# Kernel tuning notes

Measured on AMD Instinct MI355X. Metric: run time of the kernel, lower is better.

## Reference

```python
import jax, jax.numpy as jnp
import numpy as np

B, T, D, NQ, NK, H = 2, 2048, 2048, 16, 4, 128
ROPE_THETA = 10000.0

def _timescale(head_dim, max_ts=ROPE_THETA, min_ts=1.0):
    frac = 2.0 * jnp.arange(head_dim // 2, dtype=jnp.float32) / head_dim
    return (min_ts * (max_ts / min_ts) ** frac).astype(jnp.float32)

def _apply_rope(x, pos):
    # x: [B,S,N,H], pos: [B,S] int
    ts = _timescale(x.shape[-1])
    sinu = pos.astype(jnp.float32)[..., None, None] / ts  # [B,S,1,H/2]
    sin, cos = jnp.sin(sinu), jnp.cos(sinu)
    x = x.astype(jnp.float32)
    x1, x2 = jnp.split(x, 2, axis=-1)
    return jnp.concatenate((x1 * cos - x2 * sin, x2 * cos + x1 * sin), axis=-1)

def setup_inputs() -> dict:
    key = jax.random.key(0)
    ks = jax.random.split(key, 5)
    X = jax.random.normal(ks[0], (B, T, D), dtype=jnp.float32)
    q_positions = jnp.broadcast_to(jnp.arange(T, dtype=jnp.int32), (B, T))
    s = 1.0 / np.sqrt(D)
    Wq = jax.random.normal(ks[1], (D, NQ, H), dtype=jnp.float32) * s
    Wk = jax.random.normal(ks[2], (D, NK, H), dtype=jnp.float32) * s
    Wv = jax.random.normal(ks[3], (D, NK, H), dtype=jnp.float32) * s
    Wo = jax.random.normal(ks[4], (NQ, H, D), dtype=jnp.float32) * (1.0 / np.sqrt(NQ * H))
    return {"X": X, "q_positions": q_positions, "Wq": Wq, "Wk": Wk, "Wv": Wv, "Wo": Wo}

def reference(X, q_positions, Wq, Wk, Wv, Wo):
    # Q/K/V projections
    q = jnp.einsum('btd,dnh->btnh', X, Wq)   # [B,T,NQ,H]
    k = jnp.einsum('bsd,dkh->bskh', X, Wk)   # [B,S,NK,H]
    v = jnp.einsum('bsd,dkh->bskh', X, Wv)
    # RoPE (kv_positions defaults to q_positions)
    q = _apply_rope(q, q_positions)
    k = _apply_rope(k, q_positions)
    # GQA causal SDPA, scale=1.0 (as in source)
    G = NQ // NK
    qg = q.reshape(B, T, NK, G, H)
    logits = jnp.einsum('btkgh,bskh->bkgts', qg, k)  # [B,NK,G,T,S]
    t_idx = jnp.arange(T)[:, None]
    s_idx = jnp.arange(T)[None, :]
    causal = (s_idx <= t_idx)
    logits = jnp.where(causal, logits, jnp.finfo(logits.dtype).min)
    probs = jax.nn.softmax(logits, axis=-1)
    attn = jnp.einsum('bkgts,bskh->btkgh', probs, v).reshape(B, T, NQ, H)
    out = jnp.einsum('btnh,nhd->btd', attn, Wo)
    return out.astype(X.dtype)
```

## Files before the change

### kernel.cpp

```cpp
#include <hip/hip_runtime.h>


typedef _Float16 half8 __attribute__((ext_vector_type(8)));
typedef _Float16 half4 __attribute__((ext_vector_type(4)));
typedef float f32x4 __attribute__((ext_vector_type(4)));

#define GLOAD16(gp, lp) \
  __builtin_amdgcn_global_load_lds((__attribute__((address_space(1))) void*)(gp), \
                                   (__attribute__((address_space(3))) void*)(lp), 16, 0, 0)

#define WAIT_VM8() asm volatile("s_waitcnt vmcnt(8)" ::: "memory")
#define WAIT_VM0() asm volatile("s_waitcnt vmcnt(0)" ::: "memory")
#define BAR() asm volatile("s_barrier" ::: "memory")

static constexpr int T_   = 2048;
static constexpr int D_   = 2048;
static constexpr int NQ_  = 16;
static constexpr int NK_  = 4;
static constexpr int H_   = 128;
static constexpr int NQKV = 3072;
static constexpr int KOFF = 2048;
static constexpr int VOFF = 2560;


__global__ void cast_x_kernel(const float* __restrict__ in, _Float16* __restrict__ out) {
  int i = (blockIdx.x * 256 + threadIdx.x) * 4;
  float4 v = *reinterpret_cast<const float4*>(in + i);
  union { _Float16 h[4]; uint2 u; } p;
  p.h[0] = (_Float16)v.x; p.h[1] = (_Float16)v.y;
  p.h[2] = (_Float16)v.z; p.h[3] = (_Float16)v.w;
  *reinterpret_cast<uint2*>(out + i) = p.u;
}

__global__ void transpose_cast_kernel(const float* __restrict__ in,
                                      _Float16* __restrict__ out, int ncols) {
  __shared__ float tile[32][33];
  int n0 = blockIdx.x * 32, k0 = blockIdx.y * 32;
  int tx = threadIdx.x, ty = threadIdx.y;
#pragma unroll
  for (int i = 0; i < 32; i += 8)
    tile[ty + i][tx] = in[(size_t)(k0 + ty + i) * ncols + (n0 + tx)];
  __syncthreads();
#pragma unroll
  for (int i = 0; i < 32; i += 8)
    out[(size_t)(n0 + ty + i) * 2048 + (k0 + tx)] = (_Float16)tile[tx][ty + i];
}

__global__ void rope_kernel(_Float16* __restrict__ qkv, const int* __restrict__ pos) {
  int idx = blockIdx.x * 256 + threadIdx.x;
  int h = idx & 63;
  int head = (idx >> 6) % 20;
  int m = idx / (64 * 20);
  float p = (float)pos[m];
  float freq = expf(-0.14391156831f * (float)h);
  float a = p * freq;
  float s, c;
  sincosf(a, &s, &c);
  int col = (head < 16) ? (head * H_ + h) : (KOFF + (head - 16) * H_ + h);
  _Float16* ptr = qkv + (size_t)m * NQKV + col;
  float x1 = (float)ptr[0], x2 = (float)ptr[64];
  ptr[0]  = (_Float16)(x1 * c - x2 * s);
  ptr[64] = (_Float16)(x2 * c + x1 * s);
}

__global__ void vtrans_kernel(const _Float16* __restrict__ qkv, _Float16* __restrict__ vt) {
  __shared__ _Float16 tile[32][33];
  int t0 = blockIdx.x * 32, h0 = blockIdx.y * 32;
  int slab = blockIdx.z;
  int tx = threadIdx.x, ty = threadIdx.y;
  int b = slab >> 2, kh = slab & 3;
#pragma unroll
  for (int i = 0; i < 32; i += 8)
    tile[ty + i][tx] = qkv[(size_t)(b * T_ + t0 + ty + i) * NQKV + VOFF + kh * H_ + h0 + tx];
  __syncthreads();
#pragma unroll
  for (int i = 0; i < 32; i += 8)
    vt[(size_t)(slab * H_ + h0 + ty + i) * T_ + (t0 + tx)] = tile[tx][ty + i];
}


template <int OUT_F32>
__global__ __launch_bounds__(256, 2) void gemm_kernel(const _Float16* __restrict__ A,
                                                      const _Float16* __restrict__ Bt,
                                                      void* __restrict__ Cout, int N, int K) {
  __shared__ __align__(16) _Float16 As[128 * 64];
  __shared__ __align__(16) _Float16 Bs[128 * 64];
  const int tid = threadIdx.x;
  const int wave = tid >> 6, lane = tid & 63;
  const int lg = lane >> 4, lm = lane & 15;
  const int brow = blockIdx.y * 128, bcol = blockIdx.x * 128;
  const int wr = wave >> 1, wc = wave & 1;
  f32x4 acc[4][4] = {};
  for (int k0 = 0; k0 < K; k0 += 64) {
#pragma unroll
    for (int j = 0; j < 4; ++j) {
      int U = j * 256 + tid;
      int row = U >> 3, u = U & 7;
      int us = u ^ (row & 7);
      GLOAD16(A + (size_t)(brow + row) * K + k0 + us * 8, (char*)As + ((j * 256 + wave * 64) << 4));
      GLOAD16(Bt + (size_t)(bcol + row) * K + k0 + us * 8, (char*)Bs + ((j * 256 + wave * 64) << 4));
    }
    __syncthreads();
#pragma unroll
    for (int kk = 0; kk < 2; ++kk) {
      half8 af[4], bf[4];
#pragma unroll
      for (int m = 0; m < 4; ++m) {
        int row = wr * 64 + m * 16 + lm;
        int u = (kk * 4 + lg) ^ (row & 7);
        af[m] = *reinterpret_cast<const half8*>(As + row * 64 + u * 8);
      }
#pragma unroll
      for (int n = 0; n < 4; ++n) {
        int row = wc * 64 + n * 16 + lm;
        int u = (kk * 4 + lg) ^ (row & 7);
        bf[n] = *reinterpret_cast<const half8*>(Bs + row * 64 + u * 8);
      }
#pragma unroll
      for (int m = 0; m < 4; ++m)
#pragma unroll
        for (int n = 0; n < 4; ++n)
          acc[m][n] = __builtin_amdgcn_mfma_f32_16x16x32_f16(af[m], bf[n], acc[m][n], 0, 0, 0);
    }
    __syncthreads();
  }
#pragma unroll
  for (int m = 0; m < 4; ++m)
#pragma unroll
    for (int n = 0; n < 4; ++n)
#pragma unroll
      for (int r = 0; r < 4; ++r) {
        size_t row = brow + wr * 64 + m * 16 + lg * 4 + r;
        size_t col = bcol + wc * 64 + n * 16 + lm;
        if constexpr (OUT_F32) ((float*)Cout)[row * N + col] = acc[m][n][r];
        else ((_Float16*)Cout)[row * N + col] = (_Float16)acc[m][n][r];
      }
}


__global__ __launch_bounds__(256, 2) void attn_kernel(const _Float16* __restrict__ qkv,
                                                      const _Float16* __restrict__ vt,
                                                      _Float16* __restrict__ attn) {
  __shared__ __align__(16) _Float16 Ks[2][64 * 128];
  __shared__ __align__(16) _Float16 Vs[2][128 * 64];
  __shared__ __align__(16) _Float16 Ps[4][16 * 64];
  const int bid = blockIdx.x;
  const int swz = (bid & 7) * 64 + (bid >> 3);
  const int chunk = swz >> 6;
  const int b = chunk >> 2, kh = chunk & 3;
  const int n = kh * 4 + ((swz >> 4) & 3);
  const int p = swz & 15;
  const int tid = threadIdx.x, wave = tid >> 6, lane = tid & 63;
  const int lg = lane >> 4, lm = lane & 15;

  auto stage = [&](int j, int buf) {
    const int s0 = j * 64;
    char* Kb = (char*)&Ks[buf][0];
    char* Vb = (char*)&Vs[buf][0];
#pragma unroll
    for (int jj = 0; jj < 4; ++jj) {
      int U = jj * 256 + tid;
      int srow = U >> 4, u = U & 15;
      int us = u ^ (srow & 15);
      GLOAD16(qkv + (size_t)(b * T_ + s0 + srow) * NQKV + KOFF + kh * H_ + us * 8,
              Kb + ((jj * 256 + wave * 64) << 4));
    }
#pragma unroll
    for (int jj = 0; jj < 4; ++jj) {
      int U = jj * 256 + tid;
      int hrow = U >> 3, u = U & 7;
      int us = u ^ (hrow & 7);
      GLOAD16(vt + (size_t)((b * NK_ + kh) * H_ + hrow) * T_ + s0 + us * 8,
              Vb + ((jj * 256 + wave * 64) << 4));
    }
  };

  for (int ph = 0; ph < 2; ++ph) {
    const int t = ph ? (31 - p) : p;
    const int qbase = t * 64 + wave * 16;

    half8 qf[4];
    const _Float16* qptr = qkv + (size_t)(b * T_ + qbase + lm) * NQKV + n * H_;
#pragma unroll
    for (int kk = 0; kk < 4; ++kk) {
      half8 qr = *reinterpret_cast<const half8*>(qptr + kk * 32 + lg * 8);
#pragma unroll
      for (int j = 0; j < 8; ++j)
        qf[kk][j] = (_Float16)((float)qr[j] * 1.4426950408889634f);
    }

    f32x4 o[8] = {};
    float mrow_s = -1e30f, lrow_s = 0.f;

    const int nkv = t + 1;
    stage(0, 0);
    for (int it = 0; it < nkv; ++it) {
      const int cur = it & 1;
      if (it + 1 < nkv) { stage(it + 1, cur ^ 1); WAIT_VM8(); }
      else              { WAIT_VM0(); }
      BAR();
      const _Float16* Kt = &Ks[cur][0];
      const _Float16* Vt2 = &Vs[cur][0];

      f32x4 S[4];
      __builtin_amdgcn_s_setprio(1);
#pragma unroll
      for (int ns = 0; ns < 4; ++ns) {
        half8 kf[4];
        int srow = ns * 16 + lm;
#pragma unroll
        for (int kk = 0; kk < 4; ++kk) {
          int u = (kk * 4 + lg) ^ (srow & 15);
          kf[kk] = *reinterpret_cast<const half8*>(Kt + srow * 128 + u * 8);
        }
        f32x4 a = {0.f, 0.f, 0.f, 0.f};
#pragma unroll
        for (int kk = 0; kk < 4; ++kk)
          a = __builtin_amdgcn_mfma_f32_16x16x32_f16(kf[kk], qf[kk], a, 0, 0, 0);
        S[ns] = a;
      }
      __builtin_amdgcn_s_setprio(0);

      if (it == t) {
        const int q = qbase + lm;
#pragma unroll
        for (int ns = 0; ns < 4; ++ns)
#pragma unroll
          for (int r = 0; r < 4; ++r) {
            int s = t * 64 + ns * 16 + lg * 4 + r;
            if (s > q) S[ns][r] = -1e30f;
          }
      }

      float pm0 = fmaxf(fmaxf(S[0][0], S[0][1]), fmaxf(S[0][2], S[0][3]));
      float pm1 = fmaxf(fmaxf(S[1][0], S[1][1]), fmaxf(S[1][2], S[1][3]));
      float pm2 = fmaxf(fmaxf(S[2][0], S[2][1]), fmaxf(S[2][2], S[2][3]));
      float pm3 = fmaxf(fmaxf(S[3][0], S[3][1]), fmaxf(S[3][2], S[3][3]));
      float pm = fmaxf(fmaxf(pm0, pm1), fmaxf(pm2, pm3));
      pm = fmaxf(pm, __shfl_xor(pm, 16));
      pm = fmaxf(pm, __shfl_xor(pm, 32));

      if (__any(pm > mrow_s + 14.f)) {
        float mn = fmaxf(mrow_s, pm);
        float sc = __builtin_amdgcn_exp2f(mrow_s - mn);
        mrow_s = mn;
        lrow_s *= sc;
        float scr[4];
#pragma unroll
        for (int r = 0; r < 4; ++r) scr[r] = __shfl(sc, lg * 4 + r);
#pragma unroll
        for (int nh = 0; nh < 8; ++nh)
#pragma unroll
          for (int r = 0; r < 4; ++r) o[nh][r] *= scr[r];
      }

      const float m = mrow_s;
      float ps = 0.f;
#pragma unroll
      for (int ns = 0; ns < 4; ++ns)
#pragma unroll
        for (int r = 0; r < 4; ++r) {
          float pv = __builtin_amdgcn_exp2f(S[ns][r] - m);
          S[ns][r] = pv;
          ps += pv;
        }
      ps += __shfl_xor(ps, 16);
      ps += __shfl_xor(ps, 32);
      lrow_s += ps;

#pragma unroll
      for (int ns = 0; ns < 4; ++ns) {
        half4 pk;
#pragma unroll
        for (int r = 0; r < 4; ++r) pk[r] = (_Float16)S[ns][r];
        int u = (2 * ns + (lg >> 1)) ^ (lm & 7);
        *reinterpret_cast<half4*>(&Ps[wave][lm * 64 + u * 8 + (lg & 1) * 4]) = pk;
      }

      __builtin_amdgcn_s_setprio(1);
#pragma unroll
      for (int kk2 = 0; kk2 < 2; ++kk2) {
        int up = (kk2 * 4 + lg) ^ (lm & 7);
        half8 pa = *reinterpret_cast<const half8*>(&Ps[wave][lm * 64 + up * 8]);
#pragma unroll
        for (int nh = 0; nh < 8; ++nh) {
          int hrow = nh * 16 + lm;
          int u = (kk2 * 4 + lg) ^ (hrow & 7);
          half8 vf = *reinterpret_cast<const half8*>(Vt2 + hrow * 64 + u * 8);
          o[nh] = __builtin_amdgcn_mfma_f32_16x16x32_f16(pa, vf, o[nh], 0, 0, 0);
        }
      }
      __builtin_amdgcn_s_setprio(0);
      BAR();
    }

    float linv[4];
#pragma unroll
    for (int r = 0; r < 4; ++r) linv[r] = 1.f / __shfl(lrow_s, lg * 4 + r);
#pragma unroll
    for (int r = 0; r < 4; ++r) {
      int q = qbase + lg * 4 + r;
      _Float16* optr = attn + ((size_t)(b * T_ + q) * NQ_ + n) * H_ + lm;
#pragma unroll
      for (int nh = 0; nh < 8; ++nh)
        optr[nh * 16] = (_Float16)(o[nh][r] * linv[r]);
    }
  }
}


extern "C" void kernel_launch(void* const* d_in, const int* in_sizes, int n_in,
                              void* d_out, int out_size, void* d_ws, size_t ws_size,
                              hipStream_t stream) {
  const float* X  = (const float*)d_in[0];
  const int* pos  = (const int*)d_in[1];
  const float* Wq = (const float*)d_in[2];
  const float* Wk = (const float*)d_in[3];
  const float* Wv = (const float*)d_in[4];
  const float* Wo = (const float*)d_in[5];

  _Float16* Xh    = (_Float16*)d_ws;
  _Float16* Wqkvt = Xh + (size_t)4096 * 2048;
  _Float16* Wot   = Wqkvt + (size_t)3072 * 2048;
  _Float16* QKV   = Wot + (size_t)2048 * 2048;
  _Float16* Vt    = QKV + (size_t)4096 * 3072;
  _Float16* Attn  = Vt + (size_t)8 * 128 * 2048;

  dim3 tb(32, 8);
  cast_x_kernel<<<8192, 256, 0, stream>>>(X, Xh);
  transpose_cast_kernel<<<dim3(64, 64), tb, 0, stream>>>(Wq, Wqkvt, 2048);
  transpose_cast_kernel<<<dim3(16, 64), tb, 0, stream>>>(Wk, Wqkvt + (size_t)2048 * 2048, 512);
  transpose_cast_kernel<<<dim3(16, 64), tb, 0, stream>>>(Wv, Wqkvt + (size_t)2560 * 2048, 512);
  transpose_cast_kernel<<<dim3(64, 64), tb, 0, stream>>>(Wo, Wot, 2048);

  gemm_kernel<0><<<dim3(24, 32), 256, 0, stream>>>(Xh, Wqkvt, QKV, NQKV, 2048);
  rope_kernel<<<20480, 256, 0, stream>>>(QKV, pos);
  vtrans_kernel<<<dim3(64, 4, 8), tb, 0, stream>>>(QKV, Vt);
  attn_kernel<<<512, 256, 0, stream>>>(QKV, Vt, Attn);
  gemm_kernel<1><<<dim3(16, 32), 256, 0, stream>>>(Attn, Wot, d_out, 2048, 2048);
}
```

Before: 209.0 us.

## Process 32 query rows per wave in attention to reuse K/V tiles

The attention kernel now gives each wave two 16-row query sub-tiles, so each block covers 128 queries instead of 64. Every K and V fragment read from LDS then feeds twice as many MFMAs, and each staged K/V tile serves twice as many query rows. The grid is halved to 256 blocks, launch bounds drop to one block per CU, and the causal mask now applies to the last two KV tiles. The cost is higher register pressure, lower occupancy, and fewer blocks, which may leave part of the GPU idle given the causal load imbalance.

```diff
diff --git a/kernel.cpp b/kernel.cpp
--- a/kernel.cpp
+++ b/kernel.cpp
@@ -138,18 +138,18 @@
 }
 
 
-__global__ __launch_bounds__(256, 2) void attn_kernel(const _Float16* __restrict__ qkv,
+__global__ __launch_bounds__(256, 1) void attn_kernel(const _Float16* __restrict__ qkv,
                                                       const _Float16* __restrict__ vt,
                                                       _Float16* __restrict__ attn) {
   __shared__ __align__(16) _Float16 Ks[2][64 * 128];
   __shared__ __align__(16) _Float16 Vs[2][128 * 64];
-  __shared__ __align__(16) _Float16 Ps[4][16 * 64];
+  __shared__ __align__(16) _Float16 Ps[4][32 * 64];
   const int bid = blockIdx.x;
-  const int swz = (bid & 7) * 64 + (bid >> 3);
-  const int chunk = swz >> 6;
+  const int swz = (bid & 7) * 32 + (bid >> 3);
+  const int chunk = swz >> 5;
   const int b = chunk >> 2, kh = chunk & 3;
-  const int n = kh * 4 + ((swz >> 4) & 3);
-  const int p = swz & 15;
+  const int n = kh * 4 + ((swz >> 3) & 3);
+  const int p = swz & 7;
   const int tid = threadIdx.x, wave = tid >> 6, lane = tid & 63;
   const int lg = lane >> 4, lm = lane & 15;
 
@@ -176,23 +176,26 @@
   };
 
   for (int ph = 0; ph < 2; ++ph) {
-    const int t = ph ? (31 - p) : p;
-    const int qbase = t * 64 + wave * 16;
-
-    half8 qf[4];
-    const _Float16* qptr = qkv + (size_t)(b * T_ + qbase + lm) * NQKV + n * H_;
-#pragma unroll
-    for (int kk = 0; kk < 4; ++kk) {
-      half8 qr = *reinterpret_cast<const half8*>(qptr + kk * 32 + lg * 8);
-#pragma unroll
-      for (int j = 0; j < 8; ++j)
-        qf[kk][j] = (_Float16)((float)qr[j] * 1.4426950408889634f);
-    }
-
-    f32x4 o[8] = {};
-    float mrow_s = -1e30f, lrow_s = 0.f;
-
-    const int nkv = t + 1;
+    const int t = ph ? (15 - p) : p;
+    const int qbase = t * 128 + wave * 32;
+
+    half8 qf[2][4];
+#pragma unroll
+    for (int mq = 0; mq < 2; ++mq) {
+      const _Float16* qptr = qkv + (size_t)(b * T_ + qbase + mq * 16 + lm) * NQKV + n * H_;
+#pragma unroll
+      for (int kk = 0; kk < 4; ++kk) {
+        half8 qr = *reinterpret_cast<const half8*>(qptr + kk * 32 + lg * 8);
+#pragma unroll
+        for (int j = 0; j < 8; ++j)
+          qf[mq][kk][j] = (_Float16)((float)qr[j] * 1.4426950408889634f);
+      }
+    }
+
+    f32x4 o[2][8] = {};
+    float mrow[2] = {-1e30f, -1e30f}, lrow[2] = {0.f, 0.f};
+
+    const int nkv = 2 * t + 2;
     stage(0, 0);
     for (int it = 0; it < nkv; ++it) {
       const int cur = it & 1;
@@ -202,7 +205,7 @@
       const _Float16* Kt = &Ks[cur][0];
       const _Float16* Vt2 = &Vs[cur][0];
 
-      f32x4 S[4];
+      f32x4 S[2][4];
       __builtin_amdgcn_s_setprio(1);
 #pragma unroll
       for (int ns = 0; ns < 4; ++ns) {
@@ -213,97 +216,124 @@
           int u = (kk * 4 + lg) ^ (srow & 15);
           kf[kk] = *reinterpret_cast<const half8*>(Kt + srow * 128 + u * 8);
         }
-        f32x4 a = {0.f, 0.f, 0.f, 0.f};
-#pragma unroll
-        for (int kk = 0; kk < 4; ++kk)
-          a = __builtin_amdgcn_mfma_f32_16x16x32_f16(kf[kk], qf[kk], a, 0, 0, 0);
-        S[ns] = a;
+#pragma unroll
+        for (int mq = 0; mq < 2; ++mq) {
+          f32x4 a = {0.f, 0.f, 0.f, 0.f};
+#pragma unroll
+          for (int kk = 0; kk < 4; ++kk)
+            a = __builtin_amdgcn_mfma_f32_16x16x32_f16(kf[kk], qf[mq][kk], a, 0, 0, 0);
+          S[mq][ns] = a;
+        }
       }
       __builtin_amdgcn_s_setprio(0);
 
-      if (it == t) {
-        const int q = qbase + lm;
+      if (it >= 2 * t) {
+#pragma unroll
+        for (int mq = 0; mq < 2; ++mq) {
+          const int q = qbase + mq * 16 + lm;
+#pragma unroll
+          for (int ns = 0; ns < 4; ++ns)
+#pragma unroll
+            for (int r = 0; r < 4; ++r) {
+              int s = it * 64 + ns * 16 + lg * 4 + r;
+              if (s > q) S[mq][ns][r] = -1e30f;
+            }
+        }
+      }
+
+      float pm[2];
+#pragma unroll
+      for (int mq = 0; mq < 2; ++mq) {
+        float a0 = fmaxf(fmaxf(S[mq][0][0], S[mq][0][1]), fmaxf(S[mq][0][2], S[mq][0][3]));
+        float a1 = fmaxf(fmaxf(S[mq][1][0], S[mq][1][1]), fmaxf(S[mq][1][2], S[mq][1][3]));
+        float a2 = fmaxf(fmaxf(S[mq][2][0], S[mq][2][1]), fmaxf(S[mq][2][2], S[mq][2][3]));
+        float a3 = fmaxf(fmaxf(S[mq][3][0], S[mq][3][1]), fmaxf(S[mq][3][2], S[mq][3][3]));
+        float v = fmaxf(fmaxf(a0, a1), fmaxf(a2, a3));
+        v = fmaxf(v, __shfl_xor(v, 16));
+        v = fmaxf(v, __shfl_xor(v, 32));
+        pm[mq] = v;
+      }
+
+      if (__any(pm[0] > mrow[0] + 14.f || pm[1] > mrow[1] + 14.f)) {
+#pragma unroll
+        for (int mq = 0; mq < 2; ++mq) {
+          float mn = fmaxf(mrow[mq], pm[mq]);
+          float sc = __builtin_amdgcn_exp2f(mrow[mq] - mn);
+          mrow[mq] = mn;
+          lrow[mq] *= sc;
+          float scr[4];
+#pragma unroll
+          for (int r = 0; r < 4; ++r) scr[r] = __shfl(sc, lg * 4 + r);
+#pragma unroll
+          for (int nh = 0; nh < 8; ++nh)
+#pragma unroll
+            for (int r = 0; r < 4; ++r) o[mq][nh][r] *= scr[r];
+        }
+      }
+
+#pragma unroll
+      for (int mq = 0; mq < 2; ++mq) {
+        const float m = mrow[mq];
+        float ps = 0.f;
 #pragma unroll
         for (int ns = 0; ns < 4; ++ns)
 #pragma unroll
           for (int r = 0; r < 4; ++r) {
-            int s = t * 64 + ns * 16 + lg * 4 + r;
-            if (s > q) S[ns][r] = -1e30f;
+            float pv = __builtin_amdgcn_exp2f(S[mq][ns][r] - m);
+            S[mq][ns][r] = pv;
+            ps += pv;
           }
-      }
-
-      float pm0 = fmaxf(fmaxf(S[0][0], S[0][1]), fmaxf(S[0][2], S[0][3]));
-      float pm1 = fmaxf(fmaxf(S[1][0], S[1][1]), fmaxf(S[1][2], S[1][3]));
-      float pm2 = fmaxf(fmaxf(S[2][0], S[2][1]), fmaxf(S[2][2], S[2][3]));
-      float pm3 = fmaxf(fmaxf(S[3][0], S[3][1]), fmaxf(S[3][2], S[3][3]));
-      float pm = fmaxf(fmaxf(pm0, pm1), fmaxf(pm2, pm3));
-      pm = fmaxf(pm, __shfl_xor(pm, 16));
-      pm = fmaxf(pm, __shfl_xor(pm, 32));
-
-      if (__any(pm > mrow_s + 14.f)) {
-        float mn = fmaxf(mrow_s, pm);
-        float sc = __builtin_amdgcn_exp2f(mrow_s - mn);
-        mrow_s = mn;
-        lrow_s *= sc;
-        float scr[4];
-#pragma unroll
-        for (int r = 0; r < 4; ++r) scr[r] = __shfl(sc, lg * 4 + r);
-#pragma unroll
-        for (int nh = 0; nh < 8; ++nh)
-#pragma unroll
-          for (int r = 0; r < 4; ++r) o[nh][r] *= scr[r];
-      }
-
-      const float m = mrow_s;
-      float ps = 0.f;
-#pragma unroll
-      for (int ns = 0; ns < 4; ++ns)
-#pragma unroll
-        for (int r = 0; r < 4; ++r) {
-          float pv = __builtin_amdgcn_exp2f(S[ns][r] - m);
-          S[ns][r] = pv;
-          ps += pv;
-        }
-      ps += __shfl_xor(ps, 16);
-      ps += __shfl_xor(ps, 32);
-      lrow_s += ps;
-
-#pragma unroll
-      for (int ns = 0; ns < 4; ++ns) {
-        half4 pk;
-#pragma unroll
-        for (int r = 0; r < 4; ++r) pk[r] = (_Float16)S[ns][r];
-        int u = (2 * ns + (lg >> 1)) ^ (lm & 7);
-        *reinterpret_cast<half4*>(&Ps[wave][lm * 64 + u * 8 + (lg & 1) * 4]) = pk;
+        ps += __shfl_xor(ps, 16);
+        ps += __shfl_xor(ps, 32);
+        lrow[mq] += ps;
+
+        const int qq = mq * 16 + lm;
+#pragma unroll
+        for (int ns = 0; ns < 4; ++ns) {
+          half4 pk;
+#pragma unroll
+          for (int r = 0; r < 4; ++r) pk[r] = (_Float16)S[mq][ns][r];
+          int u = (2 * ns + (lg >> 1)) ^ (lm & 7);
+          *reinterpret_cast<half4*>(&Ps[wave][qq * 64 + u * 8 + (lg & 1) * 4]) = pk;
+        }
       }
 
       __builtin_amdgcn_s_setprio(1);
 #pragma unroll
       for (int kk2 = 0; kk2 < 2; ++kk2) {
-        int up = (kk2 * 4 + lg) ^ (lm & 7);
-        half8 pa = *reinterpret_cast<const half8*>(&Ps[wave][lm * 64 + up * 8]);
+        half8 pa[2];
+#pragma unroll
+        for (int mq = 0; mq < 2; ++mq) {
+          int up = (kk2 * 4 + lg) ^ (lm & 7);
+          pa[mq] = *reinterpret_cast<const half8*>(&Ps[wave][(mq * 16 + lm) * 64 + up * 8]);
+        }
 #pragma unroll
         for (int nh = 0; nh < 8; ++nh) {
           int hrow = nh * 16 + lm;
           int u = (kk2 * 4 + lg) ^ (hrow & 7);
           half8 vf = *reinterpret_cast<const half8*>(Vt2 + hrow * 64 + u * 8);
-          o[nh] = __builtin_amdgcn_mfma_f32_16x16x32_f16(pa, vf, o[nh], 0, 0, 0);
+#pragma unroll
+          for (int mq = 0; mq < 2; ++mq)
+            o[mq][nh] = __builtin_amdgcn_mfma_f32_16x16x32_f16(pa[mq], vf, o[mq][nh], 0, 0, 0);
         }
       }
       __builtin_amdgcn_s_setprio(0);
       BAR();
     }
 
-    float linv[4];
-#pragma unroll
-    for (int r = 0; r < 4; ++r) linv[r] = 1.f / __shfl(lrow_s, lg * 4 + r);
-#pragma unroll
-    for (int r = 0; r < 4; ++r) {
-      int q = qbase + lg * 4 + r;
-      _Float16* optr = attn + ((size_t)(b * T_ + q) * NQ_ + n) * H_ + lm;
-#pragma unroll
-      for (int nh = 0; nh < 8; ++nh)
-        optr[nh * 16] = (_Float16)(o[nh][r] * linv[r]);
+#pragma unroll
+    for (int mq = 0; mq < 2; ++mq) {
+      float linv[4];
+#pragma unroll
+      for (int r = 0; r < 4; ++r) linv[r] = 1.f / __shfl(lrow[mq], lg * 4 + r);
+#pragma unroll
+      for (int r = 0; r < 4; ++r) {
+        int q = qbase + mq * 16 + lg * 4 + r;
+        _Float16* optr = attn + ((size_t)(b * T_ + q) * NQ_ + n) * H_ + lm;
+#pragma unroll
+        for (int nh = 0; nh < 8; ++nh)
+          optr[nh * 16] = (_Float16)(o[mq][nh][r] * linv[r]);
+      }
     }
   }
 }
@@ -336,6 +366,6 @@
   gemm_kernel<0><<<dim3(24, 32), 256, 0, stream>>>(Xh, Wqkvt, QKV, NQKV, 2048);
   rope_kernel<<<20480, 256, 0, stream>>>(QKV, pos);
   vtrans_kernel<<<dim3(64, 4, 8), tb, 0, stream>>>(QKV, Vt);
-  attn_kernel<<<512, 256, 0, stream>>>(QKV, Vt, Attn);
+  attn_kernel<<<256, 256, 0, stream>>>(QKV, Vt, Attn);
   gemm_kernel<1><<<dim3(16, 32), 256, 0, stream>>>(Attn, Wot, d_out, 2048, 2048);
 }
```

New measurement: 222.3 us. 6.4% more time.

## Split attention into one query tile per block and single-buffer K/V for occupancy

Applied to the files above, without the earlier changes.

The attention kernel now launches 1024 blocks, each handling one 64-row query tile instead of a paired light/heavy tile. The K/V LDS double buffer is replaced by a single buffer, and launch bounds are raised so four blocks fit per CU. The aim is to hide memory latency through more resident waves rather than through software prefetch. In exchange, each iteration now waits for its own K/V load with no overlap inside a block, and load balance relies on the interleaved ordering of causal tile sizes.

```diff
diff --git a/kernel.cpp b/kernel.cpp
--- a/kernel.cpp
+++ b/kernel.cpp
@@ -9,7 +9,6 @@
   __builtin_amdgcn_global_load_lds((__attribute__((address_space(1))) void*)(gp), \
                                    (__attribute__((address_space(3))) void*)(lp), 16, 0, 0)
 
-#define WAIT_VM8() asm volatile("s_waitcnt vmcnt(8)" ::: "memory")
 #define WAIT_VM0() asm volatile("s_waitcnt vmcnt(0)" ::: "memory")
 #define BAR() asm volatile("s_barrier" ::: "memory")
 
@@ -138,32 +137,34 @@
 }
 
 
-__global__ __launch_bounds__(256, 2) void attn_kernel(const _Float16* __restrict__ qkv,
+__global__ __launch_bounds__(256, 4) void attn_kernel(const _Float16* __restrict__ qkv,
                                                       const _Float16* __restrict__ vt,
                                                       _Float16* __restrict__ attn) {
-  __shared__ __align__(16) _Float16 Ks[2][64 * 128];
-  __shared__ __align__(16) _Float16 Vs[2][128 * 64];
+  __shared__ __align__(16) _Float16 Ks[64 * 128];
+  __shared__ __align__(16) _Float16 Vs[128 * 64];
   __shared__ __align__(16) _Float16 Ps[4][16 * 64];
   const int bid = blockIdx.x;
-  const int swz = (bid & 7) * 64 + (bid >> 3);
-  const int chunk = swz >> 6;
+  const int v = (bid & 7) * 128 + (bid >> 3);
+  const int chunk = v >> 7;
   const int b = chunk >> 2, kh = chunk & 3;
-  const int n = kh * 4 + ((swz >> 4) & 3);
-  const int p = swz & 15;
+  const int j = v & 127;
+  const int h2 = j & 3;
+  const int t_raw = j >> 2;
+  const int t = (t_raw & 1) ? (31 - (t_raw >> 1)) : (t_raw >> 1);
+  const int n = kh * 4 + h2;
   const int tid = threadIdx.x, wave = tid >> 6, lane = tid & 63;
   const int lg = lane >> 4, lm = lane & 15;
-
-  auto stage = [&](int j, int buf) {
-    const int s0 = j * 64;
-    char* Kb = (char*)&Ks[buf][0];
-    char* Vb = (char*)&Vs[buf][0];
+  const int qbase = t * 64 + wave * 16;
+
+  auto stage = [&](int it) {
+    const int s0 = it * 64;
 #pragma unroll
     for (int jj = 0; jj < 4; ++jj) {
       int U = jj * 256 + tid;
       int srow = U >> 4, u = U & 15;
       int us = u ^ (srow & 15);
       GLOAD16(qkv + (size_t)(b * T_ + s0 + srow) * NQKV + KOFF + kh * H_ + us * 8,
-              Kb + ((jj * 256 + wave * 64) << 4));
+              (char*)Ks + ((jj * 256 + wave * 64) << 4));
     }
 #pragma unroll
     for (int jj = 0; jj < 4; ++jj) {
@@ -171,140 +172,132 @@
       int hrow = U >> 3, u = U & 7;
       int us = u ^ (hrow & 7);
       GLOAD16(vt + (size_t)((b * NK_ + kh) * H_ + hrow) * T_ + s0 + us * 8,
-              Vb + ((jj * 256 + wave * 64) << 4));
+              (char*)Vs + ((jj * 256 + wave * 64) << 4));
     }
   };
 
-  for (int ph = 0; ph < 2; ++ph) {
-    const int t = ph ? (31 - p) : p;
-    const int qbase = t * 64 + wave * 16;
-
-    half8 qf[4];
-    const _Float16* qptr = qkv + (size_t)(b * T_ + qbase + lm) * NQKV + n * H_;
-#pragma unroll
-    for (int kk = 0; kk < 4; ++kk) {
-      half8 qr = *reinterpret_cast<const half8*>(qptr + kk * 32 + lg * 8);
-#pragma unroll
-      for (int j = 0; j < 8; ++j)
-        qf[kk][j] = (_Float16)((float)qr[j] * 1.4426950408889634f);
-    }
-
-    f32x4 o[8] = {};
-    float mrow_s = -1e30f, lrow_s = 0.f;
-
-    const int nkv = t + 1;
-    stage(0, 0);
-    for (int it = 0; it < nkv; ++it) {
-      const int cur = it & 1;
-      if (it + 1 < nkv) { stage(it + 1, cur ^ 1); WAIT_VM8(); }
-      else              { WAIT_VM0(); }
-      BAR();
-      const _Float16* Kt = &Ks[cur][0];
-      const _Float16* Vt2 = &Vs[cur][0];
-
-      f32x4 S[4];
-      __builtin_amdgcn_s_setprio(1);
-#pragma unroll
-      for (int ns = 0; ns < 4; ++ns) {
-        half8 kf[4];
-        int srow = ns * 16 + lm;
-#pragma unroll
-        for (int kk = 0; kk < 4; ++kk) {
-          int u = (kk * 4 + lg) ^ (srow & 15);
-          kf[kk] = *reinterpret_cast<const half8*>(Kt + srow * 128 + u * 8);
+  half8 qf[4];
+  const _Float16* qptr = qkv + (size_t)(b * T_ + qbase + lm) * NQKV + n * H_;
+#pragma unroll
+  for (int kk = 0; kk < 4; ++kk) {
+    half8 qr = *reinterpret_cast<const half8*>(qptr + kk * 32 + lg * 8);
+#pragma unroll
+    for (int jj = 0; jj < 8; ++jj)
+      qf[kk][jj] = (_Float16)((float)qr[jj] * 1.4426950408889634f);
+  }
+
+  f32x4 o[8] = {};
+  float mrow_s = -1e30f, lrow_s = 0.f;
+
+  const int nkv = t + 1;
+  stage(0);
+  for (int it = 0; it < nkv; ++it) {
+    WAIT_VM0();
+    BAR();
+
+    f32x4 S[4];
+    __builtin_amdgcn_s_setprio(1);
+#pragma unroll
+    for (int ns = 0; ns < 4; ++ns) {
+      half8 kf[4];
+      int srow = ns * 16 + lm;
+#pragma unroll
+      for (int kk = 0; kk < 4; ++kk) {
+        int u = (kk * 4 + lg) ^ (srow & 15);
+        kf[kk] = *reinterpret_cast<const half8*>(Ks + srow * 128 + u * 8);
+      }
+      f32x4 a = {0.f, 0.f, 0.f, 0.f};
+#pragma unroll
+      for (int kk = 0; kk < 4; ++kk)
+        a = __builtin_amdgcn_mfma_f32_16x16x32_f16(kf[kk], qf[kk], a, 0, 0, 0);
+      S[ns] = a;
+    }
+    __builtin_amdgcn_s_setprio(0);
+
+    if (it == t) {
+      const int q = qbase + lm;
+#pragma unroll
+      for (int ns = 0; ns < 4; ++ns)
+#pragma unroll
+        for (int r = 0; r < 4; ++r) {
+          int s = t * 64 + ns * 16 + lg * 4 + r;
+          if (s > q) S[ns][r] = -1e30f;
         }
-        f32x4 a = {0.f, 0.f, 0.f, 0.f};
-#pragma unroll
-        for (int kk = 0; kk < 4; ++kk)
-          a = __builtin_amdgcn_mfma_f32_16x16x32_f16(kf[kk], qf[kk], a, 0, 0, 0);
-        S[ns] = a;
-      }
-      __builtin_amdgcn_s_setprio(0);
-
-      if (it == t) {
-        const int q = qbase + lm;
-#pragma unroll
-        for (int ns = 0; ns < 4; ++ns)
-#pragma unroll
-          for (int r = 0; r < 4; ++r) {
-            int s = t * 64 + ns * 16 + lg * 4 + r;
-            if (s > q) S[ns][r] = -1e30f;
-          }
-      }
-
-      float pm0 = fmaxf(fmaxf(S[0][0], S[0][1]), fmaxf(S[0][2], S[0][3]));
-      float pm1 = fmaxf(fmaxf(S[1][0], S[1][1]), fmaxf(S[1][2], S[1][3]));
-      float pm2 = fmaxf(fmaxf(S[2][0], S[2][1]), fmaxf(S[2][2], S[2][3]));
-      float pm3 = fmaxf(fmaxf(S[3][0], S[3][1]), fmaxf(S[3][2], S[3][3]));
-      float pm = fmaxf(fmaxf(pm0, pm1), fmaxf(pm2, pm3));
-      pm = fmaxf(pm, __shfl_xor(pm, 16));
-      pm = fmaxf(pm, __shfl_xor(pm, 32));
-
-      if (__any(pm > mrow_s + 14.f)) {
-        float mn = fmaxf(mrow_s, pm);
-        float sc = __builtin_amdgcn_exp2f(mrow_s - mn);
-        mrow_s = mn;
-        lrow_s *= sc;
-        float scr[4];
-#pragma unroll
-        for (int r = 0; r < 4; ++r) scr[r] = __shfl(sc, lg * 4 + r);
-#pragma unroll
-        for (int nh = 0; nh < 8; ++nh)
-#pragma unroll
-          for (int r = 0; r < 4; ++r) o[nh][r] *= scr[r];
-      }
-
-      const float m = mrow_s;
-      float ps = 0.f;
-#pragma unroll
-      for (int ns = 0; ns < 4; ++ns)
-#pragma unroll
-        for (int r = 0; r < 4; ++r) {
-          float pv = __builtin_amdgcn_exp2f(S[ns][r] - m);
-          S[ns][r] = pv;
-          ps += pv;
-        }
-      ps += __shfl_xor(ps, 16);
-      ps += __shfl_xor(ps, 32);
-      lrow_s += ps;
-
-#pragma unroll
-      for (int ns = 0; ns < 4; ++ns) {
-        half4 pk;
-#pragma unroll
-        for (int r = 0; r < 4; ++r) pk[r] = (_Float16)S[ns][r];
-        int u = (2 * ns + (lg >> 1)) ^ (lm & 7);
-        *reinterpret_cast<half4*>(&Ps[wave][lm * 64 + u * 8 + (lg & 1) * 4]) = pk;
-      }
-
-      __builtin_amdgcn_s_setprio(1);
-#pragma unroll
-      for (int kk2 = 0; kk2 < 2; ++kk2) {
-        int up = (kk2 * 4 + lg) ^ (lm & 7);
-        half8 pa = *reinterpret_cast<const half8*>(&Ps[wave][lm * 64 + up * 8]);
-#pragma unroll
-        for (int nh = 0; nh < 8; ++nh) {
-          int hrow = nh * 16 + lm;
-          int u = (kk2 * 4 + lg) ^ (hrow & 7);
-          half8 vf = *reinterpret_cast<const half8*>(Vt2 + hrow * 64 + u * 8);
-          o[nh] = __builtin_amdgcn_mfma_f32_16x16x32_f16(pa, vf, o[nh], 0, 0, 0);
-        }
-      }
-      __builtin_amdgcn_s_setprio(0);
-      BAR();
-    }
-
-    float linv[4];
-#pragma unroll
-    for (int r = 0; r < 4; ++r) linv[r] = 1.f / __shfl(lrow_s, lg * 4 + r);
-#pragma unroll
-    for (int r = 0; r < 4; ++r) {
-      int q = qbase + lg * 4 + r;
-      _Float16* optr = attn + ((size_t)(b * T_ + q) * NQ_ + n) * H_ + lm;
+    }
+
+    float pm0 = fmaxf(fmaxf(S[0][0], S[0][1]), fmaxf(S[0][2], S[0][3]));
+    float pm1 = fmaxf(fmaxf(S[1][0], S[1][1]), fmaxf(S[1][2], S[1][3]));
+    float pm2 = fmaxf(fmaxf(S[2][0], S[2][1]), fmaxf(S[2][2], S[2][3]));
+    float pm3 = fmaxf(fmaxf(S[3][0], S[3][1]), fmaxf(S[3][2], S[3][3]));
+    float pm = fmaxf(fmaxf(pm0, pm1), fmaxf(pm2, pm3));
+    pm = fmaxf(pm, __shfl_xor(pm, 16));
+    pm = fmaxf(pm, __shfl_xor(pm, 32));
+
+    if (__any(pm > mrow_s + 14.f)) {
+      float mn = fmaxf(mrow_s, pm);
+      float sc = __builtin_amdgcn_exp2f(mrow_s - mn);
+      mrow_s = mn;
+      lrow_s *= sc;
+      float scr[4];
+#pragma unroll
+      for (int r = 0; r < 4; ++r) scr[r] = __shfl(sc, lg * 4 + r);
 #pragma unroll
       for (int nh = 0; nh < 8; ++nh)
-        optr[nh * 16] = (_Float16)(o[nh][r] * linv[r]);
-    }
+#pragma unroll
+        for (int r = 0; r < 4; ++r) o[nh][r] *= scr[r];
+    }
+
+    const float m = mrow_s;
+    float ps = 0.f;
+#pragma unroll
+    for (int ns = 0; ns < 4; ++ns)
+#pragma unroll
+      for (int r = 0; r < 4; ++r) {
+        float pv = __builtin_amdgcn_exp2f(S[ns][r] - m);
+        S[ns][r] = pv;
+        ps += pv;
+      }
+    ps += __shfl_xor(ps, 16);
+    ps += __shfl_xor(ps, 32);
+    lrow_s += ps;
+
+#pragma unroll
+    for (int ns = 0; ns < 4; ++ns) {
+      half4 pk;
+#pragma unroll
+      for (int r = 0; r < 4; ++r) pk[r] = (_Float16)S[ns][r];
+      int u = (2 * ns + (lg >> 1)) ^ (lm & 7);
+      *reinterpret_cast<half4*>(&Ps[wave][lm * 64 + u * 8 + (lg & 1) * 4]) = pk;
+    }
+
+    __builtin_amdgcn_s_setprio(1);
+#pragma unroll
+    for (int kk2 = 0; kk2 < 2; ++kk2) {
+      int up = (kk2 * 4 + lg) ^ (lm & 7);
+      half8 pa = *reinterpret_cast<const half8*>(&Ps[wave][lm * 64 + up * 8]);
+#pragma unroll
+      for (int nh = 0; nh < 8; ++nh) {
+        int hrow = nh * 16 + lm;
+        int u = (kk2 * 4 + lg) ^ (hrow & 7);
+        half8 vf = *reinterpret_cast<const half8*>(Vs + hrow * 64 + u * 8);
+        o[nh] = __builtin_amdgcn_mfma_f32_16x16x32_f16(pa, vf, o[nh], 0, 0, 0);
+      }
+    }
+    __builtin_amdgcn_s_setprio(0);
+    BAR();
+    if (it + 1 < nkv) stage(it + 1);
+  }
+
+  float linv[4];
+#pragma unroll
+  for (int r = 0; r < 4; ++r) linv[r] = 1.f / __shfl(lrow_s, lg * 4 + r);
+#pragma unroll
+  for (int r = 0; r < 4; ++r) {
+    int q = qbase + lg * 4 + r;
+    _Float16* optr = attn + ((size_t)(b * T_ + q) * NQ_ + n) * H_ + lm;
+#pragma unroll
+    for (int nh = 0; nh < 8; ++nh)
+      optr[nh * 16] = (_Float16)(o[nh][r] * linv[r]);
   }
 }
 
@@ -336,6 +329,6 @@
   gemm_kernel<0><<<dim3(24, 32), 256, 0, stream>>>(Xh, Wqkvt, QKV, NQKV, 2048);
   rope_kernel<<<20480, 256, 0, stream>>>(QKV, pos);
   vtrans_kernel<<<dim3(64, 4, 8), tb, 0, stream>>>(QKV, Vt);
-  attn_kernel<<<512, 256, 0, stream>>>(QKV, Vt, Attn);
+  attn_kernel<<<1024, 256, 0, stream>>>(QKV, Vt, Attn);
   gemm_kernel<1><<<dim3(16, 32), 256, 0, stream>>>(Attn, Wot, d_out, 2048, 2048);
 }
```

Result: slower. 218.3 us (+4.5%).

## Replace GEMM with 256-row tiles, double-buffered LDS and XCD-aware block swizzle

Applied to the files above, without the earlier changes.

Both projection GEMMs now use a 512-thread kernel with 256xBN tiles (BN=256 for QKV, 128 for output). Global-to-LDS loads are double-buffered so the next K tile loads while the current one computes. Blocks are swizzled across the 8 XCDs, and MFMA runs are bracketed with barriers and s_setprio. Larger tiles raise data reuse and the prefetch hides load latency, at the cost of fewer blocks (192/256) and one block per CU, which may underfill 256 CUs.

```diff
diff --git a/kernel.cpp b/kernel.cpp
--- a/kernel.cpp
+++ b/kernel.cpp
@@ -79,61 +79,104 @@
 }
 
 
-template <int OUT_F32>
-__global__ __launch_bounds__(256, 2) void gemm_kernel(const _Float16* __restrict__ A,
-                                                      const _Float16* __restrict__ Bt,
-                                                      void* __restrict__ Cout, int N, int K) {
-  __shared__ __align__(16) _Float16 As[128 * 64];
-  __shared__ __align__(16) _Float16 Bs[128 * 64];
+template <int BN, int OUT_F32>
+__global__ __launch_bounds__(512, 1) void gemm256_kernel(const _Float16* __restrict__ A,
+                                                         const _Float16* __restrict__ Bt,
+                                                         void* __restrict__ Cout,
+                                                         int N, int K, int nbx) {
+  constexpr int NTN = BN / 64;
+  constexpr int MH  = (BN == 256) ? 2 : 1;
+  constexpr int MPP = 8 / MH;
+  constexpr int NLB = BN / 64;
+  __shared__ __align__(16) _Float16 As[2][256 * 64];
+  __shared__ __align__(16) _Float16 Bs[2][BN * 64];
   const int tid = threadIdx.x;
   const int wave = tid >> 6, lane = tid & 63;
   const int lg = lane >> 4, lm = lane & 15;
-  const int brow = blockIdx.y * 128, bcol = blockIdx.x * 128;
-  const int wr = wave >> 1, wc = wave & 1;
-  f32x4 acc[4][4] = {};
-  for (int k0 = 0; k0 < K; k0 += 64) {
+  const int cpx = gridDim.x >> 3;
+  const int swz = ((int)blockIdx.x & 7) * cpx + ((int)blockIdx.x >> 3);
+  const int brow = (swz / nbx) * 256, bcol = (swz % nbx) * BN;
+  const int wr = wave >> 2, wc = wave & 3;
+  constexpr int WN = BN / 4;
+  f32x4 acc[8][NTN] = {};
+  const int NT2 = K >> 6;
+
+  auto stage = [&](int kt, int buf) {
+    const int k0 = kt * 64;
 #pragma unroll
     for (int j = 0; j < 4; ++j) {
-      int U = j * 256 + tid;
+      int U = j * 512 + tid;
       int row = U >> 3, u = U & 7;
       int us = u ^ (row & 7);
-      GLOAD16(A + (size_t)(brow + row) * K + k0 + us * 8, (char*)As + ((j * 256 + wave * 64) << 4));
-      GLOAD16(Bt + (size_t)(bcol + row) * K + k0 + us * 8, (char*)Bs + ((j * 256 + wave * 64) << 4));
-    }
-    __syncthreads();
+      GLOAD16(A + (size_t)(brow + row) * K + k0 + us * 8,
+              (char*)&As[buf][0] + ((j * 512 + wave * 64) << 4));
+    }
+#pragma unroll
+    for (int j = 0; j < NLB; ++j) {
+      int U = j * 512 + tid;
+      int row = U >> 3, u = U & 7;
+      int us = u ^ (row & 7);
+      GLOAD16(Bt + (size_t)(bcol + row) * K + k0 + us * 8,
+              (char*)&Bs[buf][0] + ((j * 512 + wave * 64) << 4));
+    }
+  };
+
+  stage(0, 0);
+  stage(1, 1);
+  for (int kt = 0; kt < NT2; ++kt) {
+    const int cur = kt & 1;
+    if (kt + 1 < NT2) {
+      if constexpr (BN == 256) asm volatile("s_waitcnt vmcnt(8)" ::: "memory");
+      else                     asm volatile("s_waitcnt vmcnt(6)" ::: "memory");
+    } else {
+      WAIT_VM0();
+    }
+    BAR();
+    const _Float16* Asb = &As[cur][0];
+    const _Float16* Bsb = &Bs[cur][0];
 #pragma unroll
     for (int kk = 0; kk < 2; ++kk) {
-      half8 af[4], bf[4];
-#pragma unroll
-      for (int m = 0; m < 4; ++m) {
-        int row = wr * 64 + m * 16 + lm;
+      half8 bf[NTN];
+#pragma unroll
+      for (int nt = 0; nt < NTN; ++nt) {
+        int row = wc * WN + nt * 16 + lm;
         int u = (kk * 4 + lg) ^ (row & 7);
-        af[m] = *reinterpret_cast<const half8*>(As + row * 64 + u * 8);
-      }
-#pragma unroll
-      for (int n = 0; n < 4; ++n) {
-        int row = wc * 64 + n * 16 + lm;
-        int u = (kk * 4 + lg) ^ (row & 7);
-        bf[n] = *reinterpret_cast<const half8*>(Bs + row * 64 + u * 8);
-      }
-#pragma unroll
-      for (int m = 0; m < 4; ++m)
-#pragma unroll
-        for (int n = 0; n < 4; ++n)
-          acc[m][n] = __builtin_amdgcn_mfma_f32_16x16x32_f16(af[m], bf[n], acc[m][n], 0, 0, 0);
-    }
-    __syncthreads();
+        bf[nt] = *reinterpret_cast<const half8*>(Bsb + row * 64 + u * 8);
+      }
+#pragma unroll
+      for (int mh = 0; mh < MH; ++mh) {
+        half8 af[MPP];
+#pragma unroll
+        for (int mt = 0; mt < MPP; ++mt) {
+          int row = wr * 128 + (mh * MPP + mt) * 16 + lm;
+          int u = (kk * 4 + lg) ^ (row & 7);
+          af[mt] = *reinterpret_cast<const half8*>(Asb + row * 64 + u * 8);
+        }
+        BAR();
+        __builtin_amdgcn_s_setprio(1);
+#pragma unroll
+        for (int mt = 0; mt < MPP; ++mt)
+#pragma unroll
+          for (int nt = 0; nt < NTN; ++nt)
+            acc[mh * MPP + mt][nt] = __builtin_amdgcn_mfma_f32_16x16x32_f16(
+                af[mt], bf[nt], acc[mh * MPP + mt][nt], 0, 0, 0);
+        __builtin_amdgcn_s_setprio(0);
+        BAR();
+      }
+    }
+    if (kt + 2 < NT2) stage(kt + 2, cur);
   }
-#pragma unroll
-  for (int m = 0; m < 4; ++m)
-#pragma unroll
-    for (int n = 0; n < 4; ++n)
+
+#pragma unroll
+  for (int mt = 0; mt < 8; ++mt)
+#pragma unroll
+    for (int nt = 0; nt < NTN; ++nt)
 #pragma unroll
       for (int r = 0; r < 4; ++r) {
-        size_t row = brow + wr * 64 + m * 16 + lg * 4 + r;
-        size_t col = bcol + wc * 64 + n * 16 + lm;
-        if constexpr (OUT_F32) ((float*)Cout)[row * N + col] = acc[m][n][r];
-        else ((_Float16*)Cout)[row * N + col] = (_Float16)acc[m][n][r];
+        size_t row = brow + wr * 128 + mt * 16 + lg * 4 + r;
+        size_t col = bcol + wc * WN + nt * 16 + lm;
+        if constexpr (OUT_F32) ((float*)Cout)[row * N + col] = acc[mt][nt][r];
+        else ((_Float16*)Cout)[row * N + col] = (_Float16)acc[mt][nt][r];
       }
 }
 
@@ -333,9 +376,9 @@
   transpose_cast_kernel<<<dim3(16, 64), tb, 0, stream>>>(Wv, Wqkvt + (size_t)2560 * 2048, 512);
   transpose_cast_kernel<<<dim3(64, 64), tb, 0, stream>>>(Wo, Wot, 2048);
 
-  gemm_kernel<0><<<dim3(24, 32), 256, 0, stream>>>(Xh, Wqkvt, QKV, NQKV, 2048);
+  gemm256_kernel<256, 0><<<192, 512, 0, stream>>>(Xh, Wqkvt, QKV, NQKV, 2048, 12);
   rope_kernel<<<20480, 256, 0, stream>>>(QKV, pos);
   vtrans_kernel<<<dim3(64, 4, 8), tb, 0, stream>>>(QKV, Vt);
   attn_kernel<<<512, 256, 0, stream>>>(QKV, Vt, Attn);
-  gemm_kernel<1><<<dim3(16, 32), 256, 0, stream>>>(Attn, Wot, d_out, 2048, 2048);
-}
+  gemm256_kernel<128, 1><<<256, 512, 0, stream>>>(Attn, Wot, d_out, 2048, 2048, 16);
+}
```

Result: slower. 230.0 us (+10.1%).
